# Optimization experiments

Measured on AMD Instinct MI355X. Metric: run time of the kernel, lower is better.

The kernel has to match this reference:

```python
import jax, jax.numpy as jnp
import numpy as np

B, S, HID = 2, 2048, 1024
NH, HD = 16, 64  # op_heads, head_size; op_size = NH*HD = 1024


def setup_inputs() -> dict:
    key = jax.random.key(0)
    k1, k2, k3 = jax.random.split(key, 3)
    hidden_states = jax.random.normal(k1, (B, S, HID), dtype=jnp.float32)
    # Linear weights stored as [in, out] for x @ W + b
    Wqk = jax.random.normal(k2, (HID, 2 * NH * HD), dtype=jnp.float32) * (HID ** -0.5)
    bqk = jnp.zeros((2 * NH * HD,), dtype=jnp.float32)
    Wv = jax.random.normal(k3, (HID, NH * HD), dtype=jnp.float32) * (HID ** -0.5)
    bv = jnp.zeros((NH * HD,), dtype=jnp.float32)
    return {"hidden_states": hidden_states, "Wqk": Wqk, "bqk": bqk, "Wv": Wv, "bv": bv}


def _split_heads(t):
    # [B, S, NH*HD] -> [B, NH, S, HD]
    b, s, _ = t.shape
    return t.reshape(b, s, NH, HD).transpose(0, 2, 1, 3)


def reference(hidden_states, Wqk, bqk, Wv, bv):
    op_size = NH * HD
    qk = hidden_states @ Wqk + bqk                      # [B, S, 2*op_size]
    query, key = qk[..., :op_size], qk[..., op_size:]
    value = hidden_states @ Wv + bv                     # [B, S, op_size]
    q = _split_heads(query)                             # [B, H, S, D]
    k = _split_heads(key)
    v = _split_heads(value)
    # scores: [B, H, Sq, Sk], scaled by sqrt(head_dim) (scale_attn_weights=True)
    scores = jnp.einsum('bhqd,bhkd->bhqk', q, k) / jnp.asarray(HD ** 0.5, q.dtype)
    s = scores.shape[-1]
    causal = jnp.tril(jnp.ones((s, s), dtype=bool))     # [S, S]
    mask_value = jnp.finfo(scores.dtype).min
    scores = jnp.where(causal, scores, mask_value)
    attn = jax.nn.softmax(scores, axis=-1)              # dropout is identity (eval)
    out = jnp.einsum('bhqk,bhkd->bhqd', attn, v)        # [B, H, S, D]
    out = out.transpose(0, 2, 1, 3).reshape(out.shape[0], out.shape[2], NH * HD)
    return out
```

## Files before the change

kernel.cpp:

```cpp
#include <hip/hip_runtime.h>

typedef float floatx4 __attribute__((ext_vector_type(4)));
typedef float floatx16 __attribute__((ext_vector_type(16)));
typedef __bf16 bf16x8 __attribute__((ext_vector_type(8)));
typedef unsigned short u16x8 __attribute__((ext_vector_type(8)));
typedef unsigned short u16x4 __attribute__((ext_vector_type(4)));

#define GLDS16(g, l) __builtin_amdgcn_global_load_lds( \
    (__attribute__((address_space(1))) void*)(g), \
    (__attribute__((address_space(3))) void*)(l), 16, 0, 0)

__device__ __forceinline__ unsigned short f2bf(float f) {
    unsigned u = __float_as_uint(f);
    u += 0x7fffu + ((u >> 16) & 1u);
    return (unsigned short)(u >> 16);
}

#if __has_builtin(__builtin_amdgcn_cvt_pk_bf16_f32)
__device__ __forceinline__ unsigned pk2(float a, float b) {
    typedef __bf16 bf16x2 __attribute__((ext_vector_type(2)));
    union { bf16x2 v; unsigned u; } cv;
    cv.v = __builtin_amdgcn_cvt_pk_bf16_f32(a, b);
    return cv.u;
}
#else
__device__ __forceinline__ unsigned pk2(float a, float b) {
    return (unsigned)f2bf(a) | ((unsigned)f2bf(b) << 16);
}
#endif

#if __has_builtin(__builtin_amdgcn_exp2f)
__device__ __forceinline__ float fast_exp2(float x) { return __builtin_amdgcn_exp2f(x); }
#else
__device__ __forceinline__ float fast_exp2(float x) { return __exp2f(x); }
#endif

__global__ __launch_bounds__(256) void k_prep(const float* __restrict__ hidden,
                                              const float* __restrict__ Wqk,
                                              const float* __restrict__ Wv,
                                              unsigned short* __restrict__ Abf,
                                              unsigned short* __restrict__ Wt) {
    __shared__ unsigned short t[64][68];
    const int tid = threadIdx.x;
    if (blockIdx.x < 2048) {
        int idx = (blockIdx.x * 256 + tid) * 8;
        const float4* p = (const float4*)(hidden + idx);
        float4 f0 = p[0], f1 = p[1];
        u16x8 o;
        o[0] = f2bf(f0.x); o[1] = f2bf(f0.y); o[2] = f2bf(f0.z); o[3] = f2bf(f0.w);
        o[4] = f2bf(f1.x); o[5] = f2bf(f1.y); o[6] = f2bf(f1.z); o[7] = f2bf(f1.w);
        *(u16x8*)(Abf + idx) = o;
        return;
    }
    const int bx = blockIdx.x - 2048;
    const int n0 = (bx % 48) * 64;
    const int k0 = (bx / 48) * 64;
    const int nl = tid & 63;
    const int kb = tid >> 6;
    const int ng = n0 + nl;
#pragma unroll
    for (int i = 0; i < 16; ++i) {
        int kl = kb + i * 4;
        float v = (n0 < 2048) ? Wqk[(size_t)(k0 + kl) * 2048 + ng]
                              : Wv[(size_t)(k0 + kl) * 1024 + (ng - 2048)];
        t[nl][kl] = f2bf(v);
    }
    __syncthreads();
    const int k4 = (tid & 15) * 4;
    const int nb = tid >> 4;
#pragma unroll
    for (int i = 0; i < 4; ++i) {
        int n2 = nb + i * 16;
        u16x4 o;
        o[0] = t[n2][k4]; o[1] = t[n2][k4 + 1]; o[2] = t[n2][k4 + 2]; o[3] = t[n2][k4 + 3];
        *(u16x4*)(Wt + (size_t)(n0 + n2) * 1024 + k0 + k4) = o;
    }
}

__global__ __launch_bounds__(256, 3) void k_gemm_qkv(
    const unsigned short* __restrict__ A,
    const unsigned short* __restrict__ Bt,
    const float* __restrict__ bqk, const float* __restrict__ bvv,
    unsigned short* __restrict__ Qf, unsigned short* __restrict__ Kf,
    unsigned short* __restrict__ Vf) {
    __shared__ unsigned short As[2][128 * 32];
    __shared__ unsigned short Bs[2][128 * 32];
    const int tid = threadIdx.x;
    const int lane = tid & 63;
    const int w = tid >> 6;
    const int l15 = lane & 15;
    const int quad = lane >> 4;
    const int m0 = blockIdx.x * 128;
    const int n0 = blockIdx.y * 128;
    const int wm = (w & 1) * 64;
    const int wn = (w >> 1) * 64;
    const int rC = lane >> 2;
    const int kC = (lane & 3) * 8;
    const int c0 = w * 2;

    floatx4 acc[4][4] = {};

    const unsigned short* agp0 = A + (size_t)(m0 + c0 * 16 + rC) * 1024 + kC;
    const unsigned short* agp1 = agp0 + 16 * 1024;
    const unsigned short* bgp0 = Bt + (size_t)(n0 + c0 * 16 + rC) * 1024 + kC;
    const unsigned short* bgp1 = bgp0 + 16 * 1024;

    for (int k0 = 0; k0 < 1024; k0 += 64) {
#pragma unroll
        for (int h = 0; h < 2; ++h) {
            GLDS16(agp0 + k0 + h * 32, &As[h][c0 * 512]);
            GLDS16(agp1 + k0 + h * 32, &As[h][c0 * 512 + 512]);
            GLDS16(bgp0 + k0 + h * 32, &Bs[h][c0 * 512]);
            GLDS16(bgp1 + k0 + h * 32, &Bs[h][c0 * 512 + 512]);
        }
        __syncthreads();
#pragma unroll
        for (int h = 0; h < 2; ++h) {
            const unsigned short* ap = &As[h][(wm + l15) * 32 + quad * 8];
            const unsigned short* bp = &Bs[h][(wn + l15) * 32 + quad * 8];
            bf16x8 af[4], bfr[4];
#pragma unroll
            for (int mi = 0; mi < 4; ++mi) af[mi] = *(const bf16x8*)(ap + mi * 16 * 32);
#pragma unroll
            for (int ni = 0; ni < 4; ++ni) bfr[ni] = *(const bf16x8*)(bp + ni * 16 * 32);
#pragma unroll
            for (int mi = 0; mi < 4; ++mi)
#pragma unroll
                for (int ni = 0; ni < 4; ++ni)
                    acc[mi][ni] = __builtin_amdgcn_mfma_f32_16x16x32_bf16(af[mi], bfr[ni],
                                                                          acc[mi][ni], 0, 0, 0);
        }
        __syncthreads();
    }
#pragma unroll
    for (int ni = 0; ni < 4; ++ni) {
        const int n = n0 + wn + ni * 16 + l15;
        if (n < 2048) {
            const float bias = bqk[n];
            const bool isQ = n < 1024;
            unsigned short* dst = isQ ? Qf : Kf;
            const int hd = isQ ? n : n - 1024;
            const float scale = isQ ? 0.18033688011112042f : 1.0f;
            const int h = hd >> 6, d = hd & 63;
            const int kb = d >> 4, hhd = (d >> 3) & 1, jj = d & 7;
#pragma unroll
            for (int mi = 0; mi < 4; ++mi)
#pragma unroll
                for (int r = 0; r < 4; ++r) {
                    const int m = m0 + wm + mi * 16 + (quad << 2) + r;
                    const int b = m >> 11, s = m & 2047;
                    const int bh = b * 16 + h, t = s >> 5, cc = s & 31;
                    size_t idx = ((((size_t)(bh * 64 + t) * 4 + kb) * 2 + hhd) * 32 + cc) * 8 + jj;
                    dst[idx] = f2bf((acc[mi][ni][r] + bias) * scale);
                }
        } else {
            const float bias = bvv[n - 2048];
            const int hd = n - 2048;
            const int h = hd >> 6, d = hd & 63;
            const int dt = d >> 5, cc = d & 31;
#pragma unroll
            for (int mi = 0; mi < 4; ++mi) {
                const int m = m0 + wm + mi * 16 + (quad << 2);
                const int b = m >> 11, s = m & 2047;
                const int bh = b * 16 + h, t = s >> 5, kvr = s & 31;
                const int mb = kvr >> 4, hhv = (kvr >> 3) & 1, jj0 = s & 7;
                u16x4 o4;
#pragma unroll
                for (int r = 0; r < 4; ++r) o4[r] = f2bf(acc[mi][ni][r] + bias);
                size_t idx = (((((size_t)(bh * 64 + t) * 2 + mb) * 2 + dt) * 2 + hhv) * 32 + cc) * 8 + jj0;
                *(u16x4*)(Vf + idx) = o4;
            }
        }
    }
}

__global__ __launch_bounds__(64, 3) void k_attn(
    const unsigned short* __restrict__ Qf, const unsigned short* __restrict__ Kf,
    const unsigned short* __restrict__ Vf, float* __restrict__ out,
    float* __restrict__ Op1, float* __restrict__ l0, float* __restrict__ l1) {
    const int lane = threadIdx.x;
    const int c = lane & 31;
    const int hh = lane >> 5;
    const int gb = blockIdx.x;
    const int bh = ((gb & 7) << 2) | ((gb >> 3) & 3);
    const int u = gb >> 5;
    int j, t0, t1, mode;
    if (u < 32) { j = 63 - u; t0 = 0; t1 = 31; mode = 1; }
    else {
        const int uu = u - 32, i = uu >> 1;
        if ((uu & 1) == 0) { j = 63 - i; t0 = 32; t1 = j; mode = 2; }
        else               { j = 31 - i; t0 = 0;  t1 = j; mode = 0; }
    }
    const int q_abs = j * 32 + c;

    bf16x8 qf[4];
    {
        const unsigned short* qp = Qf + (size_t)(bh * 64 + j) * 2048 + lane * 8;
#pragma unroll
        for (int kb = 0; kb < 4; ++kb) qf[kb] = *(const bf16x8*)(qp + kb * 512);
    }
    const unsigned short* kbase = Kf + (size_t)bh * (64 * 2048) + lane * 8;
    const unsigned short* vbase = Vf + (size_t)bh * (64 * 2048) + lane * 8;

    floatx16 o2[2] = {};
    float ls0 = 0.f, ls1 = 0.f;

    bf16x8 kf[4];
    {
        const unsigned short* kp = kbase + (size_t)t0 * 2048;
#pragma unroll
        for (int kb = 0; kb < 4; ++kb) kf[kb] = *(const bf16x8*)(kp + kb * 512);
    }

    for (int t = t0; t <= t1; ++t) {
        const unsigned short* vp = vbase + (size_t)t * 2048;
        bf16x8 vf[4];
#pragma unroll
        for (int f = 0; f < 4; ++f) vf[f] = *(const bf16x8*)(vp + f * 512);

        floatx16 st = {};
#pragma unroll
        for (int kb = 0; kb < 4; ++kb)
            st = __builtin_amdgcn_mfma_f32_32x32x16_bf16(kf[kb], qf[kb], st, 0, 0, 0);

        bf16x8 kn[4];
        if (t < t1) {
            const unsigned short* kpn = kbase + (size_t)(t + 1) * 2048;
#pragma unroll
            for (int kb = 0; kb < 4; ++kb) kn[kb] = *(const bf16x8*)(kpn + kb * 512);
        }

        if (t == j) {
#pragma unroll
            for (int i = 0; i < 16; ++i) {
                const int kvr = (i & 3) + 8 * (i >> 2) + 4 * hh;
                if (kvr > c) st[i] = -1e30f;
            }
        }

        float a0 = 0.f, a1 = 0.f, a2 = 0.f, a3 = 0.f;
#pragma unroll
        for (int i = 0; i < 16; i += 4) {
            float p0 = fast_exp2(st[i + 0]);
            float p1 = fast_exp2(st[i + 1]);
            float p2 = fast_exp2(st[i + 2]);
            float p3 = fast_exp2(st[i + 3]);
            st[i + 0] = p0; st[i + 1] = p1; st[i + 2] = p2; st[i + 3] = p3;
            a0 += p0; a1 += p1; a2 += p2; a3 += p3;
        }
        ls0 += a0 + a2; ls1 += a1 + a3;

#pragma unroll
        for (int mb = 0; mb < 2; ++mb) {
            const int rb = mb * 8;
            unsigned p0 = pk2(st[rb + 0], st[rb + 1]);
            unsigned p1 = pk2(st[rb + 2], st[rb + 3]);
            unsigned p2 = pk2(st[rb + 4], st[rb + 5]);
            unsigned p3 = pk2(st[rb + 6], st[rb + 7]);
            unsigned sA = hh ? p0 : p2;
            unsigned sB = hh ? p1 : p3;
            unsigned rA = (unsigned)__shfl_xor((int)sA, 32, 64);
            unsigned rB = (unsigned)__shfl_xor((int)sB, 32, 64);
            union { unsigned u4[4]; bf16x8 v; } pf;
            if (hh == 0) { pf.u4[0] = p0; pf.u4[1] = p1; pf.u4[2] = rA; pf.u4[3] = rB; }
            else         { pf.u4[0] = rA; pf.u4[1] = rB; pf.u4[2] = p2; pf.u4[3] = p3; }
#pragma unroll
            for (int dt = 0; dt < 2; ++dt)
                o2[dt] = __builtin_amdgcn_mfma_f32_32x32x16_bf16(vf[mb * 2 + dt], pf.v,
                                                                 o2[dt], 0, 0, 0);
        }
#pragma unroll
        for (int kb = 0; kb < 4; ++kb) kf[kb] = kn[kb];
    }

    const int b = bh >> 4, head = bh & 15;
    float lrow = ls0 + ls1;
    lrow += __shfl_xor(lrow, 32, 64);
    if (mode == 0) {
        const float inv = 1.0f / lrow;
        float* op = out + (size_t)(b * 2048 + q_abs) * 1024 + head * 64;
#pragma unroll
        for (int dt = 0; dt < 2; ++dt)
#pragma unroll
            for (int rr = 0; rr < 4; ++rr) {
                float4 v4 = make_float4(o2[dt][rr * 4 + 0] * inv, o2[dt][rr * 4 + 1] * inv,
                                        o2[dt][rr * 4 + 2] * inv, o2[dt][rr * 4 + 3] * inv);
                *(float4*)(op + dt * 32 + rr * 8 + hh * 4) = v4;
            }
    } else {
        const int qr = q_abs - 1024;
        float* op;
        if (mode == 1) {
            if (hh == 0) l0[bh * 1024 + qr] = lrow;
            op = out + (size_t)(b * 2048 + q_abs) * 1024 + head * 64;
        } else {
            if (hh == 0) l1[bh * 1024 + qr] = lrow;
            op = Op1 + (size_t)(bh * 1024 + qr) * 64;
        }
#pragma unroll
        for (int dt = 0; dt < 2; ++dt)
#pragma unroll
            for (int rr = 0; rr < 4; ++rr) {
                float4 v4 = make_float4(o2[dt][rr * 4 + 0], o2[dt][rr * 4 + 1],
                                        o2[dt][rr * 4 + 2], o2[dt][rr * 4 + 3]);
                *(float4*)(op + dt * 32 + rr * 8 + hh * 4) = v4;
            }
    }
}

__global__ __launch_bounds__(256) void k_comb(const float* __restrict__ Op1,
                                              const float* __restrict__ l0,
                                              const float* __restrict__ l1,
                                              float* __restrict__ out) {
    const int idx = blockIdx.x * 256 + threadIdx.x;
    const int bh = idx >> 14;
    const int rem = idx & 16383;
    const int qr = rem >> 4;
    const int d4 = (rem & 15) << 2;
    const float inv = 1.0f / (l0[bh * 1024 + qr] + l1[bh * 1024 + qr]);
    const int b = bh >> 4, h = bh & 15;
    float* op = out + (size_t)(b * 2048 + 1024 + qr) * 1024 + h * 64 + d4;
    const float* pp = Op1 + (size_t)(bh * 1024 + qr) * 64 + d4;
    float4 a = *(const float4*)op;
    float4 p = *(const float4*)pp;
    float4 r = make_float4((a.x + p.x) * inv, (a.y + p.y) * inv,
                           (a.z + p.z) * inv, (a.w + p.w) * inv);
    *(float4*)op = r;
}

extern "C" void kernel_launch(void* const* d_in, const int* in_sizes, int n_in,
                              void* d_out, int out_size, void* d_ws, size_t ws_size,
                              hipStream_t stream) {
    const float* hidden = (const float*)d_in[0];
    const float* Wqk    = (const float*)d_in[1];
    const float* bqk    = (const float*)d_in[2];
    const float* Wv     = (const float*)d_in[3];
    const float* bvv    = (const float*)d_in[4];
    float* out = (float*)d_out;

    unsigned short* Abf = (unsigned short*)d_ws;
    unsigned short* Wt  = Abf + 4096 * 1024;
    unsigned short* Qf  = Wt + 3072 * 1024;
    unsigned short* Kf  = Qf + 32 * 2048 * 64;
    unsigned short* Vf  = Kf + 32 * 2048 * 64;
    float* Op1 = (float*)d_ws;
    float* l0  = Op1 + 32 * 1024 * 64;
    float* l1  = l0 + 32 * 1024;

    k_prep<<<2816, 256, 0, stream>>>(hidden, Wqk, Wv, Abf, Wt);
    k_gemm_qkv<<<dim3(32, 24), 256, 0, stream>>>(Abf, Wt, bqk, bvv, Qf, Kf, Vf);
    k_attn<<<3072, 64, 0, stream>>>(Qf, Kf, Vf, out, Op1, l0, l1);
    k_comb<<<2048, 256, 0, stream>>>(Op1, l0, l1, out);
}
```

Baseline: 156.6 us.

## Remap GEMM and attention blocks for XCD-local L2 reuse, pack 4 waves per block

The QKV GEMM now uses a 1D grid with a swizzle so that consecutive blocks on the same XCD share N-tiles and M-tiles, aiming to improve L2 hit rate. The attention kernel goes from 64-thread blocks to 256-thread blocks, with four waves handling four adjacent query tiles of the same head. Heads are assigned per XCD so the K/V data for a head stays in one XCD's L2. The work-ordering scheme is rebuilt around groups of four query tiles. Waves in a block now have unequal causal trip counts, so some may idle while others finish.

```diff
diff --git a/kernel.cpp b/kernel.cpp
--- a/kernel.cpp
+++ b/kernel.cpp
@@ -90,8 +90,10 @@
     const int w = tid >> 6;
     const int l15 = lane & 15;
     const int quad = lane >> 4;
-    const int m0 = blockIdx.x * 128;
-    const int n0 = blockIdx.y * 128;
+    const int gb = blockIdx.x;
+    const int q = gb >> 3;
+    const int m0 = ((((gb & 7) << 2) | (q & 3))) * 128;
+    const int n0 = (q >> 2) * 128;
     const int wm = (w & 1) * 64;
     const int wn = (w >> 1) * 64;
     const int rC = lane >> 2;
@@ -174,23 +176,30 @@
     }
 }
 
-__global__ __launch_bounds__(64, 3) void k_attn(
+__global__ __launch_bounds__(256, 3) void k_attn(
     const unsigned short* __restrict__ Qf, const unsigned short* __restrict__ Kf,
     const unsigned short* __restrict__ Vf, float* __restrict__ out,
     float* __restrict__ Op1, float* __restrict__ l0, float* __restrict__ l1) {
-    const int lane = threadIdx.x;
+    const int tid = threadIdx.x;
+    const int lane = tid & 63;
+    const int w = tid >> 6;
     const int c = lane & 31;
     const int hh = lane >> 5;
     const int gb = blockIdx.x;
-    const int bh = ((gb & 7) << 2) | ((gb >> 3) & 3);
-    const int u = gb >> 5;
-    int j, t0, t1, mode;
-    if (u < 32) { j = 63 - u; t0 = 0; t1 = 31; mode = 1; }
+    const int xcd = gb & 7;
+    const int idx = gb >> 3;
+    const int bh = xcd + ((idx & 3) << 3);
+    const int u = idx >> 2;
+    int a, mode;
+    if (u < 8) { a = 8 + u; mode = 1; }
     else {
-        const int uu = u - 32, i = uu >> 1;
-        if ((uu & 1) == 0) { j = 63 - i; t0 = 32; t1 = j; mode = 2; }
-        else               { j = 31 - i; t0 = 0;  t1 = j; mode = 0; }
-    }
+        const int i = u - 8;
+        if ((i & 1) == 0) { a = 7 - (i >> 1); mode = 0; }
+        else              { a = 15 - (i >> 1); mode = 2; }
+    }
+    const int j = 4 * a + w;
+    const int t0 = (mode == 2) ? 32 : 0;
+    const int t1 = (mode == 1) ? 31 : j;
     const int q_abs = j * 32 + c;
 
     bf16x8 qf[4];
@@ -348,7 +357,7 @@
     float* l1  = l0 + 32 * 1024;
 
     k_prep<<<2816, 256, 0, stream>>>(hidden, Wqk, Wv, Abf, Wt);
-    k_gemm_qkv<<<dim3(32, 24), 256, 0, stream>>>(Abf, Wt, bqk, bvv, Qf, Kf, Vf);
-    k_attn<<<3072, 64, 0, stream>>>(Qf, Kf, Vf, out, Op1, l0, l1);
+    k_gemm_qkv<<<768, 256, 0, stream>>>(Abf, Wt, bqk, bvv, Qf, Kf, Vf);
+    k_attn<<<768, 256, 0, stream>>>(Qf, Kf, Vf, out, Op1, l0, l1);
     k_comb<<<2048, 256, 0, stream>>>(Op1, l0, l1, out);
 }
```

Result: no change. 153.9 us (-1.7%).
